# Optimization experiments

Measured on AMD Instinct MI355X. Metric: run time of the kernel, lower is better.

Reference implementation:

```python
import jax, jax.numpy as jnp
import numpy as np

D_MODEL = 768
NUM_HEADS = 48
HEAD_CH = D_MODEL // NUM_HEADS  # 16
INNER = 3 * D_MODEL
BATCH = 2
SEQLEN = 2048
SKIP = 1.0
EPS = 1e-6


def setup_inputs() -> dict:
    key = jax.random.key(0)
    ks = jax.random.split(key, 9)
    s_in = 1.0 / np.sqrt(D_MODEL)
    s_out = 1.0 / np.sqrt(D_MODEL)
    return {
        "inputs": jax.random.normal(ks[0], (BATCH, SEQLEN, D_MODEL), jnp.float32),
        "w_in": jax.random.normal(ks[1], (INNER, D_MODEL), jnp.float32) * s_in,
        "b_in": jax.random.normal(ks[2], (INNER,), jnp.float32) * 0.01,
        "w_sf": jax.random.normal(ks[3], (INNER, 3), jnp.float32) * 0.3,  # depthwise conv kernel
        "b_sf": jax.random.normal(ks[4], (INNER,), jnp.float32) * 0.01,
        "h": jax.random.normal(ks[5], (NUM_HEADS, SEQLEN), jnp.float32) * 0.02,  # long filter
        "norm_w": jnp.ones((D_MODEL,), jnp.float32),
        "w_out": jax.random.normal(ks[6], (D_MODEL, D_MODEL), jnp.float32) * s_out,
        "b_out": jax.random.normal(ks[7], (D_MODEL,), jnp.float32) * 0.01,
    }


def reference(inputs, w_in, b_in, w_sf, b_sf, h, norm_w, w_out, b_out):
    B, L, D = inputs.shape
    N, HC = NUM_HEADS, HEAD_CH
    # in_proj: [B, L, 3D]
    u = jnp.einsum('bld,ed->ble', inputs, w_in) + b_in
    u = jnp.transpose(u, (0, 2, 1))  # [B, 3D, L]
    # causal depthwise conv1d, kernel 3, left pad 2
    up = jnp.pad(u, ((0, 0), (0, 0), (2, 0)))
    uc = (w_sf[:, 0:1] * up[:, :, 0:L]
          + w_sf[:, 1:2] * up[:, :, 1:L + 1]
          + w_sf[:, 2:3] * up[:, :, 2:L + 2]
          + b_sf[:, None])  # [B, 3D, L]
    uc = uc.reshape(B, N, 3 * HC, L)
    x0 = uc[:, :, 0:HC, :]            # q  [B, N, HC, L]
    x1 = uc[:, :, HC:2 * HC, :]       # k  [B, N, HC, L]
    v = uc[:, :, 2 * HC:3 * HC, :]    # v  [B, N, HC, L]
    # outer product: [B, HC_i, HC_j, N, L]
    kv = jnp.einsum('bnil,bnjl->bijnl', x1, v)
    # FFT long convolution with h [N, L], broadcast over b,i,j
    fft_size = 2 * L
    k_f = jnp.fft.rfft(h, n=fft_size) / fft_size        # [N, L+1]
    u_f = jnp.fft.rfft(kv, n=fft_size, axis=-1)         # [B, HC, HC, N, L+1]
    hkv = jnp.fft.irfft(u_f * k_f, n=fft_size, axis=-1, norm='forward')[..., :L]
    # contract with q: [B, L, N, HC_j]
    qhkv = jnp.einsum('bijnl,bnil->blnj', hkv, x0)
    y = qhkv.reshape(B, L, D)
    # RMSNorm
    ms = jnp.mean(jnp.square(y), axis=-1, keepdims=True)
    y = y * jax.lax.rsqrt(ms + EPS) * norm_w
    # out_proj + skip
    y = jnp.einsum('bld,ed->ble', y, w_out) + b_out
    return y + inputs * SKIP
```

## Files before the change

### kernel.cpp

```cpp
#include <hip/hip_runtime.h>
#include <hip/hip_bf16.h>
#include <stdint.h>

typedef __bf16 bf16;
typedef __bf16 bf16x4 __attribute__((ext_vector_type(4)));
typedef __bf16 bf16x8 __attribute__((ext_vector_type(8)));
typedef float f32x4 __attribute__((ext_vector_type(4)));
typedef float f32x16 __attribute__((ext_vector_type(16)));

#define D_MODEL 768
#define NUM_HEADS 48
#define HEAD_CH 16
#define INNER 2304
#define BATCH 2
#define SEQLEN 2048
#define M_ROWS (BATCH * SEQLEN)
#define EPSF 1e-6f
#define SST 40
#define HT_ROWS 2052
#define HTQ (NUM_HEADS * HT_ROWS * 4)

__device__ inline void gload_lds16(const void* g, void* l) {
  __builtin_amdgcn_global_load_lds((__attribute__((address_space(1))) void*)(g),
                                   (__attribute__((address_space(3))) void*)(l),
                                   16, 0, 0);
}

__global__ __launch_bounds__(256) void cvt2_f32_bf16(
    const float* __restrict__ a, bf16* __restrict__ da, int na4,
    const float* __restrict__ b, bf16* __restrict__ db, int nb4) {
  int j = blockIdx.x * 256 + threadIdx.x;
  const float* s;
  bf16* d;
  if (j < na4) {
    s = a; d = da;
  } else {
    j -= na4;
    if (j >= nb4) return;
    s = b; d = db;
  }
  const float4 v = ((const float4*)s)[j];
  bf16x4 o;
  o[0] = (bf16)v.x; o[1] = (bf16)v.y; o[2] = (bf16)v.z; o[3] = (bf16)v.w;
  ((bf16x4*)d)[j] = o;
}

__global__ __launch_bounds__(256) void cvt_wout_hgen(
    const float* __restrict__ wout, const float* __restrict__ nw,
    bf16* __restrict__ wout16, int n4, const float* __restrict__ hb,
    bf16* __restrict__ ht) {
  int j = blockIdx.x * 256 + threadIdx.x;
  if (j < n4) {
    const int d0 = (j * 4) % D_MODEL;
    const float4 v = ((const float4*)wout)[j];
    const float4 nv = *(const float4*)&nw[d0];
    bf16x4 o;
    o[0] = (bf16)(v.x * nv.x); o[1] = (bf16)(v.y * nv.y);
    o[2] = (bf16)(v.z * nv.z); o[3] = (bf16)(v.w * nv.w);
    ((bf16x4*)wout16)[j] = o;
    return;
  }
  j -= n4;
  if (j >= HTQ) return;
  const int nh = j / (HT_ROWS * 4);
  const int rem = j - nh * (HT_ROWS * 4);
  const int Cp = rem >> 2, rb = rem & 3;
  const float* hrow = hb + nh * SEQLEN;
  const int base = Cp - 4 - 8 * rb;
  bf16x4 o;
#pragma unroll
  for (int rr = 0; rr < 4; ++rr) {
    const int idx = base - rr;
    o[rr] = (bf16)((idx >= 0 && idx < SEQLEN) ? hrow[idx] : 0.f);
  }
  ((bf16x4*)ht)[j] = o;
}

template <int TM, int TN, int BK, int NCOLS, typename CT>
__global__ __launch_bounds__(256) void gemm_bt(
    const bf16* __restrict__ A, const bf16* __restrict__ W,
    const float* __restrict__ bias, CT* __restrict__ C, int K) {
  constexpr int MI = TM / 32;
  constexpr int NI = TN / 32;
  constexpr int KK = BK / 32;
  __shared__ __align__(16) bf16 As[TM * BK];
  __shared__ __align__(16) bf16 Bs[TN * BK];
  const int t = threadIdx.x;
  const int lane = t & 63, w = t >> 6;
  const int wm = (w >> 1) * (TM / 2), wn = (w & 1) * (TN / 2);
  const int row16 = lane & 15, quad = lane >> 4;
  const int m0 = blockIdx.x * TM, n0 = blockIdx.y * TN;

  f32x4 zero4 = {0.f, 0.f, 0.f, 0.f};
  f32x4 acc[MI][NI];
#pragma unroll
  for (int mi = 0; mi < MI; ++mi)
#pragma unroll
    for (int ni = 0; ni < NI; ++ni) acc[mi][ni] = zero4;

  const int arow = t >> 2;
  const int acol = (t & 3) * 8;
  const bf16* Ab = A + (size_t)m0 * K;
  const bf16* Wb = W + (size_t)n0 * K;

  for (int kt = 0; kt < K; kt += BK) {
#pragma unroll
    for (int kk0 = 0; kk0 < KK; ++kk0) {
#pragma unroll
      for (int rh = 0; rh < TM / 64; ++rh)
        gload_lds16(Ab + (size_t)(rh * 64 + arow) * K + kt + kk0 * 32 + acol,
                    As + kk0 * (TM * 32) + rh * 2048 + t * 8);
#pragma unroll
      for (int rh = 0; rh < TN / 64; ++rh)
        gload_lds16(Wb + (size_t)(rh * 64 + arow) * K + kt + kk0 * 32 + acol,
                    Bs + kk0 * (TN * 32) + rh * 2048 + t * 8);
    }
    __syncthreads();

    bf16x8 af[MI][KK], wf[NI][KK];
#pragma unroll
    for (int kk0 = 0; kk0 < KK; ++kk0) {
#pragma unroll
      for (int mi = 0; mi < MI; ++mi)
        af[mi][kk0] = *(const bf16x8*)&As[kk0 * (TM * 32) +
                                          (wm + mi * 16 + row16) * 32 +
                                          quad * 8];
#pragma unroll
      for (int ni = 0; ni < NI; ++ni)
        wf[ni][kk0] = *(const bf16x8*)&Bs[kk0 * (TN * 32) +
                                          (wn + ni * 16 + row16) * 32 +
                                          quad * 8];
    }
#pragma unroll
    for (int kk0 = 0; kk0 < KK; ++kk0)
#pragma unroll
      for (int mi = 0; mi < MI; ++mi)
#pragma unroll
        for (int ni = 0; ni < NI; ++ni)
          acc[mi][ni] = __builtin_amdgcn_mfma_f32_16x16x32_bf16(
              af[mi][kk0], wf[ni][kk0], acc[mi][ni], 0, 0, 0);
    __syncthreads();
  }

#pragma unroll
  for (int mi = 0; mi < MI; ++mi) {
#pragma unroll
    for (int ni = 0; ni < NI; ++ni) {
      const int col = n0 + wn + ni * 16 + row16;
      const float bv = bias[col];
#pragma unroll
      for (int r = 0; r < 4; ++r) {
        const int row = m0 + wm + mi * 16 + quad * 4 + r;
        C[(size_t)row * NCOLS + col] = (CT)(acc[mi][ni][r] + bv);
      }
    }
  }
}

__global__ __launch_bounds__(256) void gemm_rms(
    const bf16* __restrict__ A, const bf16* __restrict__ W,
    const float* __restrict__ bias, const float* __restrict__ skip,
    float* __restrict__ C) {
  constexpr int TM = 64, TN = 64, BK = 64, K = D_MODEL;
  constexpr int MI = 2, NI = 2, KK = 2;
  __shared__ __align__(16) bf16 As[TM * BK];
  __shared__ __align__(16) bf16 Bs[TN * BK];
  __shared__ float rs[TM];
  const int t = threadIdx.x;
  const int lane = t & 63, w = t >> 6;
  const int wm = (w >> 1) * 32, wn = (w & 1) * 32;
  const int row16 = lane & 15, quad = lane >> 4;
  const int m0 = blockIdx.x * TM, n0 = blockIdx.y * TN;

  f32x4 zero4 = {0.f, 0.f, 0.f, 0.f};
  f32x4 acc[MI][NI];
#pragma unroll
  for (int mi = 0; mi < MI; ++mi)
#pragma unroll
    for (int ni = 0; ni < NI; ++ni) acc[mi][ni] = zero4;

  const int arow = t >> 2;
  const int acol = (t & 3) * 8;
  const bf16* Ab = A + (size_t)m0 * K;
  const bf16* Wb = W + (size_t)n0 * K;
  float ssq = 0.f;

  for (int kt = 0; kt < K; kt += BK) {
#pragma unroll
    for (int kk0 = 0; kk0 < KK; ++kk0) {
      gload_lds16(Ab + (size_t)arow * K + kt + kk0 * 32 + acol,
                  As + kk0 * (TM * 32) + t * 8);
      gload_lds16(Wb + (size_t)arow * K + kt + kk0 * 32 + acol,
                  Bs + kk0 * (TN * 32) + t * 8);
    }
    __syncthreads();

    bf16x8 af[MI][KK], wf[NI][KK];
#pragma unroll
    for (int kk0 = 0; kk0 < KK; ++kk0) {
#pragma unroll
      for (int mi = 0; mi < MI; ++mi)
        af[mi][kk0] = *(const bf16x8*)&As[kk0 * (TM * 32) +
                                          (wm + mi * 16 + row16) * 32 +
                                          quad * 8];
#pragma unroll
      for (int ni = 0; ni < NI; ++ni)
        wf[ni][kk0] = *(const bf16x8*)&Bs[kk0 * (TN * 32) +
                                          (wn + ni * 16 + row16) * 32 +
                                          quad * 8];
    }
#pragma unroll
    for (int kk0 = 0; kk0 < KK; ++kk0) {
      const bf16x8 q =
          *(const bf16x8*)&As[kk0 * (TM * 32) + (t >> 2) * 32 + (t & 3) * 8];
#pragma unroll
      for (int jj = 0; jj < 8; ++jj) {
        const float f = (float)q[jj];
        ssq += f * f;
      }
    }
#pragma unroll
    for (int kk0 = 0; kk0 < KK; ++kk0)
#pragma unroll
      for (int mi = 0; mi < MI; ++mi)
#pragma unroll
        for (int ni = 0; ni < NI; ++ni)
          acc[mi][ni] = __builtin_amdgcn_mfma_f32_16x16x32_bf16(
              af[mi][kk0], wf[ni][kk0], acc[mi][ni], 0, 0, 0);
    __syncthreads();
  }

  float* ssr = (float*)As;
  ssr[t] = ssq;
  __syncthreads();
  if (t < TM) {
    const float s4 = ssr[4 * t] + ssr[4 * t + 1] + ssr[4 * t + 2] + ssr[4 * t + 3];
    rs[t] = rsqrtf(s4 * (1.f / (float)D_MODEL) + EPSF);
  }
  __syncthreads();

#pragma unroll
  for (int mi = 0; mi < MI; ++mi) {
#pragma unroll
    for (int ni = 0; ni < NI; ++ni) {
      const int col = n0 + wn + ni * 16 + row16;
      const float bv = bias[col];
#pragma unroll
      for (int r = 0; r < 4; ++r) {
        const int rowl = wm + mi * 16 + quad * 4 + r;
        const int row = m0 + rowl;
        C[(size_t)row * D_MODEL + col] =
            acc[mi][ni][r] * rs[rowl] + bv + skip[(size_t)row * D_MODEL + col];
      }
    }
  }
}

__global__ __launch_bounds__(256) void conv_qkv(
    const bf16* __restrict__ u, const float* __restrict__ w_sf,
    const float* __restrict__ b_sf, bf16* __restrict__ qq,
    bf16* __restrict__ kk, bf16* __restrict__ vv) {
  const int nh = blockIdx.x, b = blockIdx.y, lc = blockIdx.z;
  const int l0 = lc * 128;
  __shared__ __align__(8) bf16 ut[130 * 48];
  const int t = threadIdx.x;
  for (int i = t; i < 130 * 12; i += 256) {
    const int lr = i / 12, qd = i % 12;
    const int l = l0 - 2 + lr;
    uint2 val;
    val.x = 0u; val.y = 0u;
    if (l >= 0)
      val = *(const uint2*)&u[(size_t)(b * SEQLEN + l) * INNER + nh * 48 + qd * 4];
    *(uint2*)&ut[lr * 48 + qd * 4] = val;
  }
  __syncthreads();
  const size_t bn = (size_t)(b * NUM_HEADS + nh);
#pragma unroll
  for (int s = 0; s < 2; ++s) {
    bf16* dst = (s == 0) ? qq : kk;
    const int cb = s * 16;
    for (int i = t; i < 128 * 4; i += 256) {
      const int c4 = (i & 3) * 4, lr = i >> 2;
      const int e0 = nh * 48 + cb + c4;
      const float4 wa = *(const float4*)&w_sf[e0 * 3];
      const float4 wb = *(const float4*)&w_sf[e0 * 3 + 4];
      const float4 wc = *(const float4*)&w_sf[e0 * 3 + 8];
      const float4 bb = *(const float4*)&b_sf[e0];
      const bf16x4 u0 = *(const bf16x4*)&ut[lr * 48 + cb + c4];
      const bf16x4 u1 = *(const bf16x4*)&ut[(lr + 1) * 48 + cb + c4];
      const bf16x4 u2 = *(const bf16x4*)&ut[(lr + 2) * 48 + cb + c4];
      bf16x4 o;
      o[0] = (bf16)(wa.x * (float)u0[0] + wa.y * (float)u1[0] +
                    wa.z * (float)u2[0] + bb.x);
      o[1] = (bf16)(wa.w * (float)u0[1] + wb.x * (float)u1[1] +
                    wb.y * (float)u2[1] + bb.y);
      o[2] = (bf16)(wb.z * (float)u0[2] + wb.w * (float)u1[2] +
                    wc.x * (float)u2[2] + bb.z);
      o[3] = (bf16)(wc.y * (float)u0[3] + wc.z * (float)u1[3] +
                    wc.w * (float)u2[3] + bb.w);
      *(bf16x4*)&dst[(bn * SEQLEN + l0 + lr) * 16 + c4] = o;
    }
  }
  for (int i = t; i < 16 * 32; i += 256) {
    const int c = i >> 5, lr4 = (i & 31) * 4;
    const int e = nh * 48 + 32 + c;
    const float w0 = w_sf[e * 3 + 0], w1 = w_sf[e * 3 + 1],
                w2 = w_sf[e * 3 + 2], bv = b_sf[e];
    bf16x4 o;
#pragma unroll
    for (int k = 0; k < 4; ++k) {
      o[k] = (bf16)(w0 * (float)ut[(lr4 + k) * 48 + 32 + c] +
                    w1 * (float)ut[(lr4 + k + 1) * 48 + 32 + c] +
                    w2 * (float)ut[(lr4 + k + 2) * 48 + 32 + c] + bv);
    }
    *(bf16x4*)&vv[(bn * 16 + c) * SEQLEN + l0 + lr4] = o;
  }
}

__global__ __launch_bounds__(256) void attn_kernel(
    const bf16* __restrict__ qq, const bf16* __restrict__ kk,
    const bf16* __restrict__ vv, const bf16* __restrict__ ht,
    bf16* __restrict__ y) {
  const int nh = blockIdx.x, b = blockIdx.y;
  const int qa = blockIdx.z, qb = 63 - qa;
  const int l0a = qa * 32, l0b = qb * 32;
  __shared__ __align__(16) bf16 st[4 * 32 * SST];
  const int t = threadIdx.x;
  const int w = t >> 6, lane = t & 63;
  const int l31 = lane & 31, hi = lane >> 5;
  const int row16 = lane & 15, quad = lane >> 4;
  const size_t bn = (size_t)(b * NUM_HEADS + nh);
  const bf16* qp = qq + bn * SEQLEN * 16;
  const bf16* kb = kk + bn * SEQLEN * 16;
  const bf16* vb = vv + bn * 16 * SEQLEN;
  const bf16* hbase = ht + ((size_t)nh * HT_ROWS + (size_t)(l31 - 4 * hi + 4)) * 16;

  bf16x8 zf;
#pragma unroll
  for (int j = 0; j < 8; ++j) zf[j] = (bf16)0.f;
  const f32x4 zacc4 = {0.f, 0.f, 0.f, 0.f};
  f32x16 zacc16;
#pragma unroll
  for (int j = 0; j < 16; ++j) zacc16[j] = 0.f;

  const bf16x8 qfa = *(const bf16x8*)&qp[(l0a + l31) * 16 + hi * 8];
  const bf16x8 qfb = *(const bf16x8*)&qp[(l0b + l31) * 16 + hi * 8];

  bf16* sw = &st[w * 32 * SST];

  auto run_pass = [&](const bf16x8& qf, const int l0, const int mc0,
                      f32x4& o0, f32x4& o1) {
    int mc = mc0;
    bf16x8 kf = zf, vf = zf, hf0 = zf, hf1 = zf;
    if (mc <= l0) {
      kf = *(const bf16x8*)&kb[(mc + l31) * 16 + hi * 8];
      vf = *(const bf16x8*)&vb[row16 * SEQLEN + mc + quad * 8];
      const bf16* hp = hbase + (size_t)(l0 - mc) * 16;
      hf0 = *(const bf16x8*)hp;
      hf1 = *(const bf16x8*)(hp + 8);
    }
    for (; mc <= l0; mc += 128) {
      const int mn = mc + 128;
      bf16x8 kf2 = zf, vf2 = zf, hn0 = zf, hn1 = zf;
      if (mn <= l0) {
        kf2 = *(const bf16x8*)&kb[(mn + l31) * 16 + hi * 8];
        vf2 = *(const bf16x8*)&vb[row16 * SEQLEN + mn + quad * 8];
        const bf16* hp = hbase + (size_t)(l0 - mn) * 16;
        hn0 = *(const bf16x8*)hp;
        hn1 = *(const bf16x8*)(hp + 8);
      }
      f32x16 s =
          __builtin_amdgcn_mfma_f32_32x32x16_bf16(kf, qf, zacc16, 0, 0, 0);

#pragma unroll
      for (int g = 0; g < 4; ++g) {
        bf16x4 pk;
#pragma unroll
        for (int r = 0; r < 4; ++r) {
          const int reg = 4 * g + r;
          const float hv = (float)((g < 2) ? hf0[reg] : hf1[reg - 8]);
          pk[r] = (bf16)(s[reg] * hv);
        }
        *(bf16x4*)&sw[l31 * SST + 8 * g + 4 * hi] = pk;
      }
      asm volatile("s_waitcnt lgkmcnt(0)" ::: "memory");
      const bf16x8 sf0 = *(const bf16x8*)&sw[row16 * SST + quad * 8];
      const bf16x8 sf1 = *(const bf16x8*)&sw[(row16 + 16) * SST + quad * 8];
      o0 = __builtin_amdgcn_mfma_f32_16x16x32_bf16(sf0, vf, o0, 0, 0, 0);
      o1 = __builtin_amdgcn_mfma_f32_16x16x32_bf16(sf1, vf, o1, 0, 0, 0);
      asm volatile("" ::: "memory");
      kf = kf2; vf = vf2; hf0 = hn0; hf1 = hn1;
    }
  };

  f32x4 o0a = zacc4, o1a = zacc4, o0b = zacc4, o1b = zacc4;
  run_pass(qfa, l0a, w * 32, o0a, o1a);
  const int j0 = ((w - qa - 1) % 4 + 4) % 4;
  run_pass(qfb, l0b, j0 * 32, o0b, o1b);

  float* ob = (float*)&st[w * 32 * SST];
#pragma unroll
  for (int phase = 0; phase < 2; ++phase) {
    const f32x4& p0 = phase ? o0b : o0a;
    const f32x4& p1 = phase ? o1b : o1a;
    const int lt = phase ? l0b : l0a;
    __syncthreads();
#pragma unroll
    for (int r = 0; r < 4; ++r) {
      ob[(quad * 4 + r) * 16 + row16] = p0[r];
      ob[(quad * 4 + r + 16) * 16 + row16] = p1[r];
    }
    __syncthreads();
    for (int i = t; i < 32 * 16; i += 256) {
      const int l = i >> 4, j = i & 15;
      float sum = 0.f;
#pragma unroll
      for (int ww = 0; ww < 4; ++ww)
        sum += ((const float*)&st[ww * 32 * SST])[l * 16 + j];
      y[((size_t)(b * SEQLEN + lt + l) * NUM_HEADS + nh) * 16 + j] = (bf16)sum;
    }
  }
}

extern "C" void kernel_launch(void* const* d_in, const int* in_sizes, int n_in,
                              void* d_out, int out_size, void* d_ws,
                              size_t ws_size, hipStream_t stream) {
  const float* inputs = (const float*)d_in[0];
  const float* w_in = (const float*)d_in[1];
  const float* b_in = (const float*)d_in[2];
  const float* w_sf = (const float*)d_in[3];
  const float* b_sf = (const float*)d_in[4];
  const float* hb = (const float*)d_in[5];
  const float* norm_w = (const float*)d_in[6];
  const float* w_out = (const float*)d_in[7];
  const float* b_out = (const float*)d_in[8];

  char* ws = (char*)d_ws;
  const size_t U_B = (size_t)M_ROWS * INNER * 2;
  const size_t V_B = (size_t)BATCH * NUM_HEADS * HEAD_CH * SEQLEN * 2;
  const size_t SLOT_B = (size_t)M_ROWS * D_MODEL * 2;
  bf16* u = (bf16*)(ws);
  bf16* wout16 = (bf16*)(ws);
  bf16* ht = (bf16*)(ws + (2 << 20));
  bf16* y16 = (bf16*)(ws + (9 << 20));
  bf16* v = (bf16*)(ws + U_B);
  bf16* in16 = (bf16*)(ws + U_B + V_B);
  bf16* k16 = in16;
  bf16* win16 = (bf16*)(ws + U_B + V_B + SLOT_B);
  bf16* q16 = win16;
  float* out = (float*)d_out;

  const int n4_in = M_ROWS * D_MODEL / 4;
  const int n4_win = INNER * D_MODEL / 4;
  const int n4_wout = D_MODEL * D_MODEL / 4;
  hipLaunchKernelGGL(cvt2_f32_bf16, dim3((n4_in + n4_win + 255) / 256),
                     dim3(256), 0, stream, inputs, in16, n4_in, w_in, win16,
                     n4_win);

  hipLaunchKernelGGL((gemm_bt<128, 128, 64, INNER, bf16>), dim3(32, 18),
                     dim3(256), 0, stream, in16, win16, b_in, u, 768);
  hipLaunchKernelGGL(conv_qkv, dim3(48, 2, 16), dim3(256), 0, stream, u, w_sf,
                     b_sf, q16, k16, v);
  hipLaunchKernelGGL(cvt_wout_hgen, dim3((n4_wout + HTQ + 255) / 256),
                     dim3(256), 0, stream, w_out, norm_w, wout16, n4_wout, hb,
                     ht);
  hipLaunchKernelGGL(attn_kernel, dim3(48, 2, 32), dim3(256), 0, stream, q16,
                     k16, v, ht, y16);
  hipLaunchKernelGGL(gemm_rms, dim3(64, 12), dim3(256), 0, stream, y16, wout16,
                     b_out, inputs, out);
}
```

Measured before the change: 192.6 us.

## Stage long filter in LDS, add XCD swizzle to GEMMs, scalarize conv

After: 182.2 us. 5.4% less time.

```diff
diff --git a/kernel.cpp b/kernel.cpp
--- a/kernel.cpp
+++ b/kernel.cpp
@@ -17,13 +17,20 @@
 #define M_ROWS (BATCH * SEQLEN)
 #define EPSF 1e-6f
 #define SST 40
-#define HT_ROWS 2052
-#define HTQ (NUM_HEADS * HT_ROWS * 4)
 
 __device__ inline void gload_lds16(const void* g, void* l) {
   __builtin_amdgcn_global_load_lds((__attribute__((address_space(1))) void*)(g),
                                    (__attribute__((address_space(3))) void*)(l),
                                    16, 0, 0);
+}
+
+__device__ inline void xcd_swz(int& bx, int& by) {
+  const int nx = gridDim.x;
+  const int f = bx + nx * by;
+  const int q = (nx * gridDim.y) >> 3;
+  const int s = (f & 7) * q + (f >> 3);
+  bx = s % nx;
+  by = s / nx;
 }
 
 __global__ __launch_bounds__(256) void cvt2_f32_bf16(
@@ -45,35 +52,19 @@
   ((bf16x4*)d)[j] = o;
 }
 
-__global__ __launch_bounds__(256) void cvt_wout_hgen(
-    const float* __restrict__ wout, const float* __restrict__ nw,
-    bf16* __restrict__ wout16, int n4, const float* __restrict__ hb,
-    bf16* __restrict__ ht) {
-  int j = blockIdx.x * 256 + threadIdx.x;
-  if (j < n4) {
-    const int d0 = (j * 4) % D_MODEL;
-    const float4 v = ((const float4*)wout)[j];
+__global__ __launch_bounds__(256) void cvt_wout_nw(
+    const float* __restrict__ src, const float* __restrict__ nw,
+    bf16* __restrict__ dst, int n4) {
+  const int i = blockIdx.x * 256 + threadIdx.x;
+  if (i < n4) {
+    const int d0 = (i * 4) % D_MODEL;
+    const float4 v = ((const float4*)src)[i];
     const float4 nv = *(const float4*)&nw[d0];
     bf16x4 o;
     o[0] = (bf16)(v.x * nv.x); o[1] = (bf16)(v.y * nv.y);
     o[2] = (bf16)(v.z * nv.z); o[3] = (bf16)(v.w * nv.w);
-    ((bf16x4*)wout16)[j] = o;
-    return;
-  }
-  j -= n4;
-  if (j >= HTQ) return;
-  const int nh = j / (HT_ROWS * 4);
-  const int rem = j - nh * (HT_ROWS * 4);
-  const int Cp = rem >> 2, rb = rem & 3;
-  const float* hrow = hb + nh * SEQLEN;
-  const int base = Cp - 4 - 8 * rb;
-  bf16x4 o;
-#pragma unroll
-  for (int rr = 0; rr < 4; ++rr) {
-    const int idx = base - rr;
-    o[rr] = (bf16)((idx >= 0 && idx < SEQLEN) ? hrow[idx] : 0.f);
-  }
-  ((bf16x4*)ht)[j] = o;
+    ((bf16x4*)dst)[i] = o;
+  }
 }
 
 template <int TM, int TN, int BK, int NCOLS, typename CT>
@@ -89,7 +80,9 @@
   const int lane = t & 63, w = t >> 6;
   const int wm = (w >> 1) * (TM / 2), wn = (w & 1) * (TN / 2);
   const int row16 = lane & 15, quad = lane >> 4;
-  const int m0 = blockIdx.x * TM, n0 = blockIdx.y * TN;
+  int bx = blockIdx.x, by = blockIdx.y;
+  xcd_swz(bx, by);
+  const int m0 = bx * TM, n0 = by * TN;
 
   f32x4 zero4 = {0.f, 0.f, 0.f, 0.f};
   f32x4 acc[MI][NI];
@@ -170,7 +163,9 @@
   const int lane = t & 63, w = t >> 6;
   const int wm = (w >> 1) * 32, wn = (w & 1) * 32;
   const int row16 = lane & 15, quad = lane >> 4;
-  const int m0 = blockIdx.x * TM, n0 = blockIdx.y * TN;
+  int bx = blockIdx.x, by = blockIdx.y;
+  xcd_swz(bx, by);
+  const int m0 = bx * TM, n0 = by * TN;
 
   f32x4 zero4 = {0.f, 0.f, 0.f, 0.f};
   f32x4 acc[MI][NI];
@@ -279,53 +274,45 @@
   for (int s = 0; s < 2; ++s) {
     bf16* dst = (s == 0) ? qq : kk;
     const int cb = s * 16;
-    for (int i = t; i < 128 * 4; i += 256) {
-      const int c4 = (i & 3) * 4, lr = i >> 2;
-      const int e0 = nh * 48 + cb + c4;
-      const float4 wa = *(const float4*)&w_sf[e0 * 3];
-      const float4 wb = *(const float4*)&w_sf[e0 * 3 + 4];
-      const float4 wc = *(const float4*)&w_sf[e0 * 3 + 8];
-      const float4 bb = *(const float4*)&b_sf[e0];
-      const bf16x4 u0 = *(const bf16x4*)&ut[lr * 48 + cb + c4];
-      const bf16x4 u1 = *(const bf16x4*)&ut[(lr + 1) * 48 + cb + c4];
-      const bf16x4 u2 = *(const bf16x4*)&ut[(lr + 2) * 48 + cb + c4];
-      bf16x4 o;
-      o[0] = (bf16)(wa.x * (float)u0[0] + wa.y * (float)u1[0] +
-                    wa.z * (float)u2[0] + bb.x);
-      o[1] = (bf16)(wa.w * (float)u0[1] + wb.x * (float)u1[1] +
-                    wb.y * (float)u2[1] + bb.y);
-      o[2] = (bf16)(wb.z * (float)u0[2] + wb.w * (float)u1[2] +
-                    wc.x * (float)u2[2] + bb.z);
-      o[3] = (bf16)(wc.y * (float)u0[3] + wc.z * (float)u1[3] +
-                    wc.w * (float)u2[3] + bb.w);
-      *(bf16x4*)&dst[(bn * SEQLEN + l0 + lr) * 16 + c4] = o;
-    }
-  }
-  for (int i = t; i < 16 * 32; i += 256) {
-    const int c = i >> 5, lr4 = (i & 31) * 4;
+    for (int i = t; i < 128 * 16; i += 256) {
+      const int c = i & 15, lr = i >> 4;
+      const int e = nh * 48 + cb + c;
+      const float val = w_sf[e * 3 + 0] * (float)ut[lr * 48 + cb + c] +
+                        w_sf[e * 3 + 1] * (float)ut[(lr + 1) * 48 + cb + c] +
+                        w_sf[e * 3 + 2] * (float)ut[(lr + 2) * 48 + cb + c] +
+                        b_sf[e];
+      dst[(bn * SEQLEN + l0 + lr) * 16 + c] = (bf16)val;
+    }
+  }
+  for (int i = t; i < 128 * 16; i += 256) {
+    const int lr = i & 127, c = i >> 7;
     const int e = nh * 48 + 32 + c;
-    const float w0 = w_sf[e * 3 + 0], w1 = w_sf[e * 3 + 1],
-                w2 = w_sf[e * 3 + 2], bv = b_sf[e];
-    bf16x4 o;
-#pragma unroll
-    for (int k = 0; k < 4; ++k) {
-      o[k] = (bf16)(w0 * (float)ut[(lr4 + k) * 48 + 32 + c] +
-                    w1 * (float)ut[(lr4 + k + 1) * 48 + 32 + c] +
-                    w2 * (float)ut[(lr4 + k + 2) * 48 + 32 + c] + bv);
-    }
-    *(bf16x4*)&vv[(bn * 16 + c) * SEQLEN + l0 + lr4] = o;
+    const float val = w_sf[e * 3 + 0] * (float)ut[lr * 48 + 32 + c] +
+                      w_sf[e * 3 + 1] * (float)ut[(lr + 1) * 48 + 32 + c] +
+                      w_sf[e * 3 + 2] * (float)ut[(lr + 2) * 48 + 32 + c] +
+                      b_sf[e];
+    vv[(bn * 16 + c) * SEQLEN + l0 + lr] = (bf16)val;
   }
 }
 
 __global__ __launch_bounds__(256) void attn_kernel(
     const bf16* __restrict__ qq, const bf16* __restrict__ kk,
-    const bf16* __restrict__ vv, const bf16* __restrict__ ht,
+    const bf16* __restrict__ vv, const float* __restrict__ hg,
     bf16* __restrict__ y) {
   const int nh = blockIdx.x, b = blockIdx.y;
   const int qa = blockIdx.z, qb = 63 - qa;
   const int l0a = qa * 32, l0b = qb * 32;
+  __shared__ __align__(16) float hs[32 + SEQLEN];
   __shared__ __align__(16) bf16 st[4 * 32 * SST];
   const int t = threadIdx.x;
+  const int n4 = (l0b + 64) >> 2;
+  for (int i = t; i < n4; i += 256) {
+    float4 val = {0.f, 0.f, 0.f, 0.f};
+    if (i >= 8) val = ((const float4*)(hg + nh * SEQLEN))[i - 8];
+    ((float4*)hs)[i] = val;
+  }
+  __syncthreads();
+
   const int w = t >> 6, lane = t & 63;
   const int l31 = lane & 31, hi = lane >> 5;
   const int row16 = lane & 15, quad = lane >> 4;
@@ -333,7 +320,6 @@
   const bf16* qp = qq + bn * SEQLEN * 16;
   const bf16* kb = kk + bn * SEQLEN * 16;
   const bf16* vb = vv + bn * 16 * SEQLEN;
-  const bf16* hbase = ht + ((size_t)nh * HT_ROWS + (size_t)(l31 - 4 * hi + 4)) * 16;
 
   bf16x8 zf;
 #pragma unroll
@@ -351,36 +337,30 @@
   auto run_pass = [&](const bf16x8& qf, const int l0, const int mc0,
                       f32x4& o0, f32x4& o1) {
     int mc = mc0;
-    bf16x8 kf = zf, vf = zf, hf0 = zf, hf1 = zf;
+    bf16x8 kf = zf, vf = zf;
     if (mc <= l0) {
       kf = *(const bf16x8*)&kb[(mc + l31) * 16 + hi * 8];
       vf = *(const bf16x8*)&vb[row16 * SEQLEN + mc + quad * 8];
-      const bf16* hp = hbase + (size_t)(l0 - mc) * 16;
-      hf0 = *(const bf16x8*)hp;
-      hf1 = *(const bf16x8*)(hp + 8);
     }
     for (; mc <= l0; mc += 128) {
       const int mn = mc + 128;
-      bf16x8 kf2 = zf, vf2 = zf, hn0 = zf, hn1 = zf;
+      bf16x8 kf2 = zf, vf2 = zf;
       if (mn <= l0) {
         kf2 = *(const bf16x8*)&kb[(mn + l31) * 16 + hi * 8];
         vf2 = *(const bf16x8*)&vb[row16 * SEQLEN + mn + quad * 8];
-        const bf16* hp = hbase + (size_t)(l0 - mn) * 16;
-        hn0 = *(const bf16x8*)hp;
-        hn1 = *(const bf16x8*)(hp + 8);
       }
       f32x16 s =
           __builtin_amdgcn_mfma_f32_32x32x16_bf16(kf, qf, zacc16, 0, 0, 0);
 
+      const int d0 = 32 + (l0 - mc) + l31 - 4 * hi;
 #pragma unroll
       for (int g = 0; g < 4; ++g) {
+        const float* hp = &hs[d0 - 8 * g - 3];
         bf16x4 pk;
-#pragma unroll
-        for (int r = 0; r < 4; ++r) {
-          const int reg = 4 * g + r;
-          const float hv = (float)((g < 2) ? hf0[reg] : hf1[reg - 8]);
-          pk[r] = (bf16)(s[reg] * hv);
-        }
+        pk[0] = (bf16)(s[4 * g + 0] * hp[3]);
+        pk[1] = (bf16)(s[4 * g + 1] * hp[2]);
+        pk[2] = (bf16)(s[4 * g + 2] * hp[1]);
+        pk[3] = (bf16)(s[4 * g + 3] * hp[0]);
         *(bf16x4*)&sw[l31 * SST + 8 * g + 4 * hi] = pk;
       }
       asm volatile("s_waitcnt lgkmcnt(0)" ::: "memory");
@@ -389,7 +369,7 @@
       o0 = __builtin_amdgcn_mfma_f32_16x16x32_bf16(sf0, vf, o0, 0, 0, 0);
       o1 = __builtin_amdgcn_mfma_f32_16x16x32_bf16(sf1, vf, o1, 0, 0, 0);
       asm volatile("" ::: "memory");
-      kf = kf2; vf = vf2; hf0 = hn0; hf1 = hn1;
+      kf = kf2; vf = vf2;
     }
   };
 
@@ -441,7 +421,6 @@
   const size_t SLOT_B = (size_t)M_ROWS * D_MODEL * 2;
   bf16* u = (bf16*)(ws);
   bf16* wout16 = (bf16*)(ws);
-  bf16* ht = (bf16*)(ws + (2 << 20));
   bf16* y16 = (bf16*)(ws + (9 << 20));
   bf16* v = (bf16*)(ws + U_B);
   bf16* in16 = (bf16*)(ws + U_B + V_B);
@@ -461,11 +440,10 @@
                      dim3(256), 0, stream, in16, win16, b_in, u, 768);
   hipLaunchKernelGGL(conv_qkv, dim3(48, 2, 16), dim3(256), 0, stream, u, w_sf,
                      b_sf, q16, k16, v);
-  hipLaunchKernelGGL(cvt_wout_hgen, dim3((n4_wout + HTQ + 255) / 256),
-                     dim3(256), 0, stream, w_out, norm_w, wout16, n4_wout, hb,
-                     ht);
+  hipLaunchKernelGGL(cvt_wout_nw, dim3((n4_wout + 255) / 256), dim3(256), 0,
+                     stream, w_out, norm_w, wout16, n4_wout);
   hipLaunchKernelGGL(attn_kernel, dim3(48, 2, 32), dim3(256), 0, stream, q16,
-                     k16, v, ht, y16);
+                     k16, v, hb, y16);
   hipLaunchKernelGGL(gemm_rms, dim3(64, 12), dim3(256), 0, stream, y16, wout16,
                      b_out, inputs, out);
 }
```
